# Optimization experiments

Measured on AMD Instinct MI355X. Metric: run time of the kernel, lower is better.

## Reference

```python
import jax, jax.numpy as jnp
import numpy as np

N_NODES = 50000
N_EDGES = 800000
D = 128


def setup_inputs() -> dict:
    key = jax.random.key(0)
    ks = jax.random.split(key, 8)
    h = jax.random.normal(ks[0], (N_NODES, D), dtype=jnp.float32)
    src = jax.random.randint(ks[1], (N_EDGES,), 0, N_NODES, dtype=jnp.int64)
    dst = jax.random.randint(ks[2], (N_EDGES,), 0, N_NODES, dtype=jnp.int64)
    # Glorot-ish init for the three GraphConv weights
    scale = 1.0 / np.sqrt(D)
    W0 = jax.random.normal(ks[3], (D, D), dtype=jnp.float32) * scale
    W1 = jax.random.normal(ks[4], (D, D), dtype=jnp.float32) * scale
    W2 = jax.random.normal(ks[5], (D, D), dtype=jnp.float32) * scale
    b0 = jnp.zeros((D,), dtype=jnp.float32)
    b1 = jnp.zeros((D,), dtype=jnp.float32)
    b2 = jnp.zeros((D,), dtype=jnp.float32)
    return {"h": h, "src": src, "dst": dst, "W0": W0, "b0": b0,
            "W1": W1, "b1": b1, "W2": W2, "b2": b2}


def _graph_conv(x, src, dst, W, b, n_nodes):
    """DGL GraphConv, norm='both', activation=ReLU.
    in_feats == out_feats -> aggregate first, then matmul W."""
    ones = jnp.ones_like(src, dtype=x.dtype)
    out_deg = jnp.clip(jax.ops.segment_sum(ones, src, num_segments=n_nodes), 1.0)
    in_deg = jnp.clip(jax.ops.segment_sum(ones, dst, num_segments=n_nodes), 1.0)
    x = x * (out_deg ** -0.5)[:, None]          # src-side normalization
    m = jax.ops.segment_sum(x[src], dst, num_segments=n_nodes)  # sparse aggregation
    m = m * (in_deg ** -0.5)[:, None]           # dst-side normalization
    return jax.nn.relu(m @ W + b)


def reference(h, src, dst, W0, b0, W1, b1, W2, b2):
    n = h.shape[0]
    h = _graph_conv(h, src, dst, W0, b0, n)
    h = _graph_conv(h, src, dst, W1, b1, n)
    h = _graph_conv(h, src, dst, W2, b2, n)
    return h
```

## Files before the change

### kernel.cpp

```cpp
#include <hip/hip_runtime.h>

#define N_NODES 50000
#define N_EDGES 800000
#define D 128
#define CAP 48
#define MS_STRIDE 132

#define NPART 625
#define EPB   (N_EDGES / NPART)
#define NRANGE 8
#define RNODES (N_NODES / NRANGE)
#define FILLGRID (NPART * NRANGE)

#define SBLK ((N_NODES + 255) / 256)

typedef __attribute__((ext_vector_type(4))) float f32x4;
typedef __attribute__((ext_vector_type(8))) short s16x8;

__device__ inline unsigned short f32_to_bf16_rtne(float f) {
    union { float f; unsigned u; } c; c.f = f;
    unsigned u = c.u;
    u += 0x7FFF + ((u >> 16) & 1);
    return (unsigned short)(u >> 16);
}
__device__ inline float bf16_to_f32(unsigned short h) {
    union { unsigned u; float f; } c; c.u = ((unsigned)h) << 16;
    return c.f;
}
__device__ inline unsigned pack_bf2(float a, float b) {
    return (unsigned)f32_to_bf16_rtne(a) | ((unsigned)f32_to_bf16_rtne(b) << 16);
}
__device__ inline void unpack_bf2(unsigned u, float& a, float& b) {
    union { unsigned u; float f; } c0, c1;
    c0.u = u << 16; c1.u = u & 0xFFFF0000u;
    a = c0.f; b = c1.f;
}
__device__ inline void acc_uint4(uint4 v, float* a) {
    float f0, f1;
    unpack_bf2(v.x, f0, f1); a[0] += f0; a[1] += f1;
    unpack_bf2(v.y, f0, f1); a[2] += f0; a[3] += f1;
    unpack_bf2(v.z, f0, f1); a[4] += f0; a[5] += f1;
    unpack_bf2(v.w, f0, f1); a[6] += f0; a[7] += f1;
}


__global__ __launch_bounds__(256) void build_fill(const int* __restrict__ src,
                                                  const int* __restrict__ dst,
                                                  int* __restrict__ cursor,
                                                  int* __restrict__ odeg,
                                                  unsigned short* __restrict__ slots) {
    int b = blockIdx.x;
    int r = b & (NRANGE - 1);
    int p = b >> 3;
    int n0 = r * RNODES;
    int e0 = p * EPB;
    for (int i = threadIdx.x; i < EPB; i += 256) {
        int e = e0 + i;
        int s = src[e];
        int d = dst[e];
        if ((unsigned)(s - n0) < (unsigned)RNODES)
            atomicAdd(&odeg[s], 1);
        if ((unsigned)(d - n0) < (unsigned)RNODES) {
            int pos = atomicAdd(&cursor[d], 1);
            if (pos < CAP) slots[d * CAP + pos] = (unsigned short)s;
        }
    }
}


__global__ __launch_bounds__(256) void mid_pack(const int* __restrict__ odeg,
                                                float* __restrict__ s_out,
                                                const float* __restrict__ W0,
                                                const float* __restrict__ W1,
                                                const float* __restrict__ W2,
                                                s16x8* __restrict__ wpk) {
    int blk = blockIdx.x;
    if (blk < SBLK) {
        int i = blk * 256 + threadIdx.x;
        if (i < N_NODES) s_out[i] = rsqrtf(fmaxf((float)odeg[i], 1.0f));
    } else {
        int wid = (blk - SBLK) * 4 + (threadIdx.x >> 6);
        if (wid >= 96) return;
        int lane = threadIdx.x & 63;
        int layer = wid / 32, rem = wid % 32;
        int ct = rem >> 2, ks = rem & 3;
        const float* W = (layer == 0) ? W0 : (layer == 1) ? W1 : W2;
        int col = ct * 16 + (lane & 15);
        int k0  = ks * 32 + (lane >> 4) * 8;
        s16x8 hi, lo;
#pragma unroll
        for (int j = 0; j < 8; j++) {
            float w = W[(k0 + j) * D + col];
            unsigned short h = f32_to_bf16_rtne(w);
            hi[j] = (short)h;
            lo[j] = (short)f32_to_bf16_rtne(w - bf16_to_f32(h));
        }
        int idx = layer * 4096 + (ct * 4 + ks) * 64 + lane;
        wpk[idx]        = hi;
        wpk[idx + 2048] = lo;
    }
}


__global__ __launch_bounds__(256) void hconv(const float4* __restrict__ h,
                                             const float* __restrict__ s_out,
                                             uint2* __restrict__ hbA,
                                             uint2* __restrict__ hbB) {
    int gid = blockIdx.x * 256 + threadIdx.x;
    const int total = N_NODES * 32;
    if (gid < total) {
        float so = s_out[gid >> 5];
        float4 v = h[gid];
        hbA[gid] = make_uint2(pack_bf2(so * v.x, so * v.y), pack_bf2(so * v.z, so * v.w));
    } else if (gid < total + 32) {
        hbA[total + (gid - total)] = make_uint2(0u, 0u);
    } else if (gid < total + 64) {
        hbB[total + (gid - total - 32)] = make_uint2(0u, 0u);
    }
}


__global__ __launch_bounds__(256) void fused_layer(const uint4* __restrict__ x,
                                                   const unsigned short* __restrict__ slots,
                                                   const int* __restrict__ deg,
                                                   const s16x8* __restrict__ wpk,
                                                   const float* __restrict__ bias,
                                                   const float* __restrict__ s_out,
                                                   float* __restrict__ outf,
                                                   unsigned short* __restrict__ outb) {
    __shared__ float mS[16 * MS_STRIDE];
    int tid = threadIdx.x;
    int row0 = blockIdx.x * 16;

    {
        int nloc = tid >> 4;
        int l    = tid & 15;
        int node = row0 + nloc;
        int dgraw = deg[node];
        int dg = min(dgraw, CAP);
        int base = node * CAP;
        int idx0 = (l      < dg) ? (int)slots[base + l]      : N_NODES;
        int idx1 = (16 + l < dg) ? (int)slots[base + 16 + l] : N_NODES;
        int idx2 = (32 + l < dg) ? (int)slots[base + 32 + l] : N_NODES;

        float a[8];
#pragma unroll
        for (int j = 0; j < 8; j++) a[j] = 0.f;

        int nr = (dg + 7) >> 3;
        for (int r = 0; r < nr; r++) {
            int c = r >> 1;
            int v = (c == 0) ? idx0 : ((c == 1) ? idx1 : idx2);
            int k = (r & 1) * 8;
            int s0 = __shfl(v, k + 0, 16), s1 = __shfl(v, k + 1, 16);
            int s2 = __shfl(v, k + 2, 16), s3 = __shfl(v, k + 3, 16);
            int s4 = __shfl(v, k + 4, 16), s5 = __shfl(v, k + 5, 16);
            int s6 = __shfl(v, k + 6, 16), s7 = __shfl(v, k + 7, 16);
            uint4 g0 = x[s0 * 16 + l];
            uint4 g1 = x[s1 * 16 + l];
            uint4 g2 = x[s2 * 16 + l];
            uint4 g3 = x[s3 * 16 + l];
            uint4 g4 = x[s4 * 16 + l];
            uint4 g5 = x[s5 * 16 + l];
            uint4 g6 = x[s6 * 16 + l];
            uint4 g7 = x[s7 * 16 + l];
            acc_uint4(g0, a); acc_uint4(g1, a); acc_uint4(g2, a); acc_uint4(g3, a);
            acc_uint4(g4, a); acc_uint4(g5, a); acc_uint4(g6, a); acc_uint4(g7, a);
        }
        float si = rsqrtf(fmaxf((float)dgraw, 1.0f));
        float* dp = &mS[nloc * MS_STRIDE + l * 8];
#pragma unroll
        for (int j = 0; j < 8; j++) dp[j] = a[j] * si;
    }
    __syncthreads();

    int wv = tid >> 6;
    int lane = tid & 63;
    int arow = lane & 15, aq = lane >> 4;
    int ct0 = wv * 2, ct1 = ct0 + 1;
    f32x4 acc0 = (f32x4)0.f, acc1 = (f32x4)0.f;

#pragma unroll
    for (int ks = 0; ks < 4; ks++) {
        const float* ap = &mS[arow * MS_STRIDE + ks * 32 + aq * 8];
        s16x8 ahi, alo;
#pragma unroll
        for (int j = 0; j < 8; j++) {
            float av = ap[j];
            unsigned short hh = f32_to_bf16_rtne(av);
            ahi[j] = (short)hh;
            alo[j] = (short)f32_to_bf16_rtne(av - bf16_to_f32(hh));
        }
        int idx0 = (ct0 * 4 + ks) * 64 + lane;
        int idx1 = (ct1 * 4 + ks) * 64 + lane;
        s16x8 b0h = wpk[idx0], b0l = wpk[idx0 + 2048];
        s16x8 b1h = wpk[idx1], b1l = wpk[idx1 + 2048];
        acc0 = __builtin_amdgcn_mfma_f32_16x16x32_bf16(ahi, b0h, acc0, 0, 0, 0);
        acc0 = __builtin_amdgcn_mfma_f32_16x16x32_bf16(alo, b0h, acc0, 0, 0, 0);
        acc0 = __builtin_amdgcn_mfma_f32_16x16x32_bf16(ahi, b0l, acc0, 0, 0, 0);
        acc1 = __builtin_amdgcn_mfma_f32_16x16x32_bf16(ahi, b1h, acc1, 0, 0, 0);
        acc1 = __builtin_amdgcn_mfma_f32_16x16x32_bf16(alo, b1h, acc1, 0, 0, 0);
        acc1 = __builtin_amdgcn_mfma_f32_16x16x32_bf16(ahi, b1l, acc1, 0, 0, 0);
    }

    int crow0 = aq * 4;
    float so4[4];
    if (outb) {
#pragma unroll
        for (int r = 0; r < 4; r++) so4[r] = s_out[row0 + crow0 + r];
    }
    int colA = ct0 * 16 + arow, colB = ct1 * 16 + arow;
    float bA = bias[colA], bB = bias[colB];
#pragma unroll
    for (int r = 0; r < 4; r++) {
        size_t rowoff = (size_t)(row0 + crow0 + r) * D;
        float vA = fmaxf(acc0[r] + bA, 0.f);
        float vB = fmaxf(acc1[r] + bB, 0.f);
        if (outf) { outf[rowoff + colA] = vA; outf[rowoff + colB] = vB; }
        if (outb) {
            outb[rowoff + colA] = f32_to_bf16_rtne(so4[r] * vA);
            outb[rowoff + colB] = f32_to_bf16_rtne(so4[r] * vB);
        }
    }
}


extern "C" void kernel_launch(void* const* d_in, const int* in_sizes, int n_in,
                              void* d_out, int out_size, void* d_ws, size_t ws_size,
                              hipStream_t stream) {
    const float* h  = (const float*)d_in[0];
    const int*  src = (const int*)d_in[1];
    const int*  dst = (const int*)d_in[2];
    const float* W0 = (const float*)d_in[3];
    const float* b0 = (const float*)d_in[4];
    const float* W1 = (const float*)d_in[5];
    const float* b1 = (const float*)d_in[6];
    const float* W2 = (const float*)d_in[7];
    const float* b2 = (const float*)d_in[8];
    float* out = (float*)d_out;

    char* w = (char*)d_ws;
    auto carve = [&](size_t bytes) -> void* {
        void* p = (void*)w;
        w += (bytes + 255) & ~(size_t)255;
        return p;
    };
    int*      cursor  = (int*)carve(2 * N_NODES * sizeof(int));
    int*      odeg    = cursor + N_NODES;
    float*    s_out   = (float*)carve(N_NODES * sizeof(float));
    unsigned short* slots = (unsigned short*)carve((size_t)N_NODES * CAP * sizeof(unsigned short));
    unsigned short* actA  = (unsigned short*)carve((size_t)(N_NODES + 1) * D * 2);
    unsigned short* actB  = (unsigned short*)carve((size_t)(N_NODES + 1) * D * 2);
    s16x8*    wpk     = (s16x8*)carve(3 * 4096 * sizeof(s16x8));

    hipMemsetAsync(cursor, 0, 2 * N_NODES * sizeof(int), stream);
    build_fill<<<FILLGRID, 256, 0, stream>>>(src, dst, cursor, odeg, slots);
    mid_pack<<<SBLK + 24, 256, 0, stream>>>(odeg, s_out, W0, W1, W2, wpk);
    hconv<<<(N_NODES * 32 + 64 + 255) / 256, 256, 0, stream>>>((const float4*)h, s_out,
                                                               (uint2*)actA, (uint2*)actB);

    const int GRID = N_NODES / 16;

    fused_layer<<<GRID, 256, 0, stream>>>((const uint4*)actA, slots, cursor,
                                          wpk, b0, s_out, nullptr, actB);
    fused_layer<<<GRID, 256, 0, stream>>>((const uint4*)actB, slots, cursor,
                                          wpk + 4096, b1, s_out, nullptr, actA);
    fused_layer<<<GRID, 256, 0, stream>>>((const uint4*)actA, slots, cursor,
                                          wpk + 8192, b2, s_out, out, nullptr);
}
```

Before: 262.2 us.

## Use XCC-aware work queues in graph build, fold weight pack and norm compute

The CSR-slot build kernel now hands edge partitions out through per-node-range atomic queues, and each block starts on the range matching its XCC id so that atomics to a given node range tend to stay within one XCC's L2. The weight packing work moves into the build kernel as extra blocks, and the out-degree normalization is computed inside hconv, which removes the mid_pack launch. This adds atomic queue traffic and relies on XCC_ID hardware register semantics. Work balance across XCCs becomes dynamic.

```diff
diff --git a/kernel.cpp b/kernel.cpp
--- a/kernel.cpp
+++ b/kernel.cpp
@@ -10,9 +10,8 @@
 #define EPB   (N_EDGES / NPART)
 #define NRANGE 8
 #define RNODES (N_NODES / NRANGE)
-#define FILLGRID (NPART * NRANGE)
-
-#define SBLK ((N_NODES + 255) / 256)
+#define QBLKS  4096
+#define PACKB  24
 
 typedef __attribute__((ext_vector_type(4))) float f32x4;
 typedef __attribute__((ext_vector_type(8))) short s16x8;
@@ -48,38 +47,15 @@
                                                   const int* __restrict__ dst,
                                                   int* __restrict__ cursor,
                                                   int* __restrict__ odeg,
-                                                  unsigned short* __restrict__ slots) {
+                                                  int* __restrict__ qheads,
+                                                  unsigned short* __restrict__ slots,
+                                                  const float* __restrict__ W0,
+                                                  const float* __restrict__ W1,
+                                                  const float* __restrict__ W2,
+                                                  s16x8* __restrict__ wpk) {
     int b = blockIdx.x;
-    int r = b & (NRANGE - 1);
-    int p = b >> 3;
-    int n0 = r * RNODES;
-    int e0 = p * EPB;
-    for (int i = threadIdx.x; i < EPB; i += 256) {
-        int e = e0 + i;
-        int s = src[e];
-        int d = dst[e];
-        if ((unsigned)(s - n0) < (unsigned)RNODES)
-            atomicAdd(&odeg[s], 1);
-        if ((unsigned)(d - n0) < (unsigned)RNODES) {
-            int pos = atomicAdd(&cursor[d], 1);
-            if (pos < CAP) slots[d * CAP + pos] = (unsigned short)s;
-        }
-    }
-}
-
-
-__global__ __launch_bounds__(256) void mid_pack(const int* __restrict__ odeg,
-                                                float* __restrict__ s_out,
-                                                const float* __restrict__ W0,
-                                                const float* __restrict__ W1,
-                                                const float* __restrict__ W2,
-                                                s16x8* __restrict__ wpk) {
-    int blk = blockIdx.x;
-    if (blk < SBLK) {
-        int i = blk * 256 + threadIdx.x;
-        if (i < N_NODES) s_out[i] = rsqrtf(fmaxf((float)odeg[i], 1.0f));
-    } else {
-        int wid = (blk - SBLK) * 4 + (threadIdx.x >> 6);
+    if (b >= QBLKS) {
+        int wid = (b - QBLKS) * 4 + (threadIdx.x >> 6);
         if (wid >= 96) return;
         int lane = threadIdx.x & 63;
         int layer = wid / 32, rem = wid % 32;
@@ -98,18 +74,51 @@
         int idx = layer * 4096 + (ct * 4 + ks) * 64 + lane;
         wpk[idx]        = hi;
         wpk[idx + 2048] = lo;
+        return;
+    }
+
+    int myx;
+    asm volatile("s_getreg_b32 %0, hwreg(HW_REG_XCC_ID)" : "=s"(myx));
+    myx &= (NRANGE - 1);
+
+    __shared__ int sp;
+    for (int rr = 0; rr < NRANGE; rr++) {
+        int r = (myx + rr) & (NRANGE - 1);
+        int n0 = r * RNODES;
+        for (;;) {
+            if (threadIdx.x == 0) sp = atomicAdd(&qheads[r], 1);
+            __syncthreads();
+            int p = sp;
+            if (p >= NPART) break;
+            int e0 = p * EPB;
+            for (int i = threadIdx.x; i < EPB; i += 256) {
+                int e = e0 + i;
+                int s = src[e];
+                int d = dst[e];
+                if ((unsigned)(s - n0) < (unsigned)RNODES)
+                    atomicAdd(&odeg[s], 1);
+                if ((unsigned)(d - n0) < (unsigned)RNODES) {
+                    int pos = atomicAdd(&cursor[d], 1);
+                    if (pos < CAP) slots[d * CAP + pos] = (unsigned short)s;
+                }
+            }
+            __syncthreads();
+        }
     }
 }
 
 
 __global__ __launch_bounds__(256) void hconv(const float4* __restrict__ h,
-                                             const float* __restrict__ s_out,
+                                             const int* __restrict__ odeg,
+                                             float* __restrict__ s_out,
                                              uint2* __restrict__ hbA,
                                              uint2* __restrict__ hbB) {
     int gid = blockIdx.x * 256 + threadIdx.x;
     const int total = N_NODES * 32;
     if (gid < total) {
-        float so = s_out[gid >> 5];
+        int node = gid >> 5;
+        float so = rsqrtf(fmaxf((float)odeg[node], 1.0f));
+        if ((gid & 31) == 0) s_out[node] = so;
         float4 v = h[gid];
         hbA[gid] = make_uint2(pack_bf2(so * v.x, so * v.y), pack_bf2(so * v.z, so * v.w));
     } else if (gid < total + 32) {
@@ -245,18 +254,19 @@
         w += (bytes + 255) & ~(size_t)255;
         return p;
     };
-    int*      cursor  = (int*)carve(2 * N_NODES * sizeof(int));
+    int*      cursor  = (int*)carve((2 * N_NODES + NRANGE) * sizeof(int));
     int*      odeg    = cursor + N_NODES;
+    int*      qheads  = cursor + 2 * N_NODES;
     float*    s_out   = (float*)carve(N_NODES * sizeof(float));
     unsigned short* slots = (unsigned short*)carve((size_t)N_NODES * CAP * sizeof(unsigned short));
     unsigned short* actA  = (unsigned short*)carve((size_t)(N_NODES + 1) * D * 2);
     unsigned short* actB  = (unsigned short*)carve((size_t)(N_NODES + 1) * D * 2);
     s16x8*    wpk     = (s16x8*)carve(3 * 4096 * sizeof(s16x8));
 
-    hipMemsetAsync(cursor, 0, 2 * N_NODES * sizeof(int), stream);
-    build_fill<<<FILLGRID, 256, 0, stream>>>(src, dst, cursor, odeg, slots);
-    mid_pack<<<SBLK + 24, 256, 0, stream>>>(odeg, s_out, W0, W1, W2, wpk);
-    hconv<<<(N_NODES * 32 + 64 + 255) / 256, 256, 0, stream>>>((const float4*)h, s_out,
+    hipMemsetAsync(cursor, 0, (2 * N_NODES + NRANGE) * sizeof(int), stream);
+    build_fill<<<QBLKS + PACKB, 256, 0, stream>>>(src, dst, cursor, odeg, qheads, slots,
+                                                  W0, W1, W2, wpk);
+    hconv<<<(N_NODES * 32 + 64 + 255) / 256, 256, 0, stream>>>((const float4*)h, odeg, s_out,
                                                                (uint2*)actA, (uint2*)actB);
 
     const int GRID = N_NODES / 16;
```

Result: slower. 658.3 us (+151.1%).

## Flatten edge fill to one thread per edge and fuse setup kernels

Applied to the files above, without the earlier changes.

Replaces the partitioned, range-filtered fill (each edge read once per node range) with one thread per edge doing direct atomics. Slot writes use atomicOr on 32-bit words, which requires zeroing the slot buffer first. The weight packing moves into the fill kernel and the out-degree normalization into the conversion kernel, removing one launch. The cost is an extra memset and less locality in the atomic updates.

```diff
diff --git a/kernel.cpp b/kernel.cpp
--- a/kernel.cpp
+++ b/kernel.cpp
@@ -6,13 +6,8 @@
 #define CAP 48
 #define MS_STRIDE 132
 
-#define NPART 625
-#define EPB   (N_EDGES / NPART)
-#define NRANGE 8
-#define RNODES (N_NODES / NRANGE)
-#define FILLGRID (NPART * NRANGE)
-
-#define SBLK ((N_NODES + 255) / 256)
+#define FILLB (N_EDGES / 256)
+#define PACKB 24
 
 typedef __attribute__((ext_vector_type(4))) float f32x4;
 typedef __attribute__((ext_vector_type(8))) short s16x8;
@@ -48,38 +43,23 @@
                                                   const int* __restrict__ dst,
                                                   int* __restrict__ cursor,
                                                   int* __restrict__ odeg,
-                                                  unsigned short* __restrict__ slots) {
+                                                  unsigned* __restrict__ slots32,
+                                                  const float* __restrict__ W0,
+                                                  const float* __restrict__ W1,
+                                                  const float* __restrict__ W2,
+                                                  s16x8* __restrict__ wpk) {
     int b = blockIdx.x;
-    int r = b & (NRANGE - 1);
-    int p = b >> 3;
-    int n0 = r * RNODES;
-    int e0 = p * EPB;
-    for (int i = threadIdx.x; i < EPB; i += 256) {
-        int e = e0 + i;
+    if (b < FILLB) {
+        int e = b * 256 + threadIdx.x;
         int s = src[e];
         int d = dst[e];
-        if ((unsigned)(s - n0) < (unsigned)RNODES)
-            atomicAdd(&odeg[s], 1);
-        if ((unsigned)(d - n0) < (unsigned)RNODES) {
-            int pos = atomicAdd(&cursor[d], 1);
-            if (pos < CAP) slots[d * CAP + pos] = (unsigned short)s;
-        }
-    }
-}
-
-
-__global__ __launch_bounds__(256) void mid_pack(const int* __restrict__ odeg,
-                                                float* __restrict__ s_out,
-                                                const float* __restrict__ W0,
-                                                const float* __restrict__ W1,
-                                                const float* __restrict__ W2,
-                                                s16x8* __restrict__ wpk) {
-    int blk = blockIdx.x;
-    if (blk < SBLK) {
-        int i = blk * 256 + threadIdx.x;
-        if (i < N_NODES) s_out[i] = rsqrtf(fmaxf((float)odeg[i], 1.0f));
+        atomicAdd(&odeg[s], 1);
+        int pos = atomicAdd(&cursor[d], 1);
+        if (pos < CAP)
+            atomicOr(&slots32[d * (CAP / 2) + (pos >> 1)],
+                     ((unsigned)(unsigned short)s) << ((pos & 1) * 16));
     } else {
-        int wid = (blk - SBLK) * 4 + (threadIdx.x >> 6);
+        int wid = (b - FILLB) * 4 + (threadIdx.x >> 6);
         if (wid >= 96) return;
         int lane = threadIdx.x & 63;
         int layer = wid / 32, rem = wid % 32;
@@ -103,13 +83,16 @@
 
 
 __global__ __launch_bounds__(256) void hconv(const float4* __restrict__ h,
-                                             const float* __restrict__ s_out,
+                                             const int* __restrict__ odeg,
+                                             float* __restrict__ s_out,
                                              uint2* __restrict__ hbA,
                                              uint2* __restrict__ hbB) {
     int gid = blockIdx.x * 256 + threadIdx.x;
     const int total = N_NODES * 32;
     if (gid < total) {
-        float so = s_out[gid >> 5];
+        int node = gid >> 5;
+        float so = rsqrtf(fmaxf((float)odeg[node], 1.0f));
+        if ((gid & 31) == 0) s_out[node] = so;
         float4 v = h[gid];
         hbA[gid] = make_uint2(pack_bf2(so * v.x, so * v.y), pack_bf2(so * v.z, so * v.w));
     } else if (gid < total + 32) {
@@ -248,23 +231,24 @@
     int*      cursor  = (int*)carve(2 * N_NODES * sizeof(int));
     int*      odeg    = cursor + N_NODES;
     float*    s_out   = (float*)carve(N_NODES * sizeof(float));
-    unsigned short* slots = (unsigned short*)carve((size_t)N_NODES * CAP * sizeof(unsigned short));
+    unsigned* slots32 = (unsigned*)carve((size_t)N_NODES * CAP * sizeof(unsigned short));
     unsigned short* actA  = (unsigned short*)carve((size_t)(N_NODES + 1) * D * 2);
     unsigned short* actB  = (unsigned short*)carve((size_t)(N_NODES + 1) * D * 2);
     s16x8*    wpk     = (s16x8*)carve(3 * 4096 * sizeof(s16x8));
 
     hipMemsetAsync(cursor, 0, 2 * N_NODES * sizeof(int), stream);
-    build_fill<<<FILLGRID, 256, 0, stream>>>(src, dst, cursor, odeg, slots);
-    mid_pack<<<SBLK + 24, 256, 0, stream>>>(odeg, s_out, W0, W1, W2, wpk);
-    hconv<<<(N_NODES * 32 + 64 + 255) / 256, 256, 0, stream>>>((const float4*)h, s_out,
+    hipMemsetAsync(slots32, 0, (size_t)N_NODES * CAP * sizeof(unsigned short), stream);
+    build_fill<<<FILLB + PACKB, 256, 0, stream>>>(src, dst, cursor, odeg, slots32,
+                                                  W0, W1, W2, wpk);
+    hconv<<<(N_NODES * 32 + 64 + 255) / 256, 256, 0, stream>>>((const float4*)h, odeg, s_out,
                                                                (uint2*)actA, (uint2*)actB);
 
     const int GRID = N_NODES / 16;
 
-    fused_layer<<<GRID, 256, 0, stream>>>((const uint4*)actA, slots, cursor,
-                                          wpk, b0, s_out, nullptr, actB);
-    fused_layer<<<GRID, 256, 0, stream>>>((const uint4*)actB, slots, cursor,
-                                          wpk + 4096, b1, s_out, nullptr, actA);
-    fused_layer<<<GRID, 256, 0, stream>>>((const uint4*)actA, slots, cursor,
-                                          wpk + 8192, b2, s_out, out, nullptr);
-}
+    fused_layer<<<GRID, 256, 0, stream>>>((const uint4*)actA, (const unsigned short*)slots32,
+                                          cursor, wpk, b0, s_out, nullptr, actB);
+    fused_layer<<<GRID, 256, 0, stream>>>((const uint4*)actB, (const unsigned short*)slots32,
+                                          cursor, wpk + 4096, b1, s_out, nullptr, actA);
+    fused_layer<<<GRID, 256, 0, stream>>>((const uint4*)actA, (const unsigned short*)slots32,
+                                          cursor, wpk + 8192, b2, s_out, out, nullptr);
+}
```

After: 293.6 us. 1.12x slower.
